# Kernel optimization log

Hardware: AMD Instinct MI355X
Metric: run time of the kernel (lower is better)

Reference implementation:

```python
import jax, jax.numpy as jnp
import numpy as np

TEMP = 1.0
EPS = 1e-6


def trop_linear(x, w, b, temp=TEMP):
    # x: (..., in), w: (out, in) -> (..., out)
    # y_i = temp * logsumexp_j((w_ij + x_j)/temp) + b_i  (soft tropical / max-plus)
    z = x[..., None, :] + w  # (..., out, in)
    y = temp * jax.nn.logsumexp(z / temp, axis=-1)
    return y + b


def trop_layernorm(x, weight, bias, eps=EPS):
    n = x.shape[-1]
    # torch.median returns the lower of the two middle elements for even n
    med = jnp.sort(x, axis=-1)[..., (n - 1) // 2][..., None]
    q75 = jnp.quantile(x, 0.75, axis=-1, keepdims=True)
    q25 = jnp.quantile(x, 0.25, axis=-1, keepdims=True)
    iqr = jnp.maximum(q75 - q25, eps)
    return (x - med) / iqr * weight + bias


def setup_inputs() -> dict:
    key = jax.random.key(0)
    ks = jax.random.split(key, 8)
    B, D_IN, D_H, D_OUT = 1024, 512, 512, 256
    return {
        "x": jax.random.normal(ks[0], (B, D_IN), dtype=jnp.float32),
        "w1": 0.1 * jax.random.normal(ks[1], (D_H, D_IN), dtype=jnp.float32),
        "b1": jnp.zeros((D_H,), dtype=jnp.float32),
        "ln1_w": jnp.ones((D_H,), dtype=jnp.float32),
        "ln1_b": jnp.zeros((D_H,), dtype=jnp.float32),
        "w2": 0.1 * jax.random.normal(ks[2], (D_H, D_H), dtype=jnp.float32),
        "b2": jnp.zeros((D_H,), dtype=jnp.float32),
        "ln2_w": jnp.ones((D_H,), dtype=jnp.float32),
        "ln2_b": jnp.zeros((D_H,), dtype=jnp.float32),
        "w3": 0.1 * jax.random.normal(ks[3], (D_OUT, D_H), dtype=jnp.float32),
        "b3": jnp.zeros((D_OUT,), dtype=jnp.float32),
    }


def reference(x, w1, b1, ln1_w, ln1_b, w2, b2, ln2_w, ln2_b, w3, b3):
    h = trop_linear(x, w1, b1)
    h = trop_layernorm(h, ln1_w, ln1_b)
    h = jnp.maximum(h, 0.0)  # TropicalActivation('relu', threshold=0)
    h = trop_linear(h, w2, b2)
    h = trop_layernorm(h, ln2_w, ln2_b)
    h = jnp.maximum(h, 0.0)
    return trop_linear(h, w3, b3)
```

## Files before the change

### kernel.cpp

```cpp
#include <hip/hip_runtime.h>
#include <math.h>


typedef _Float16 v8h __attribute__((ext_vector_type(8)));
typedef _Float16 v4h __attribute__((ext_vector_type(4)));
typedef float v4f __attribute__((ext_vector_type(4)));

#define ELS_STRIDE 528

__global__ __launch_bounds__(256) void expW_frag(const float* __restrict__ w1,
                                                 const float* __restrict__ w2,
                                                 const float* __restrict__ w3,
                                                 _Float16* __restrict__ Ef) {
    int u = blockIdx.x * 256 + threadIdx.x;
    int lane = u & 63, t = (u >> 6) & 15, S = u >> 10;
    int r = lane & 15, q = lane >> 4;
    const float* w; int tile;
    if (S < 32)      { w = w1; tile = S; }
    else if (S < 64) { w = w2; tile = S - 32; }
    else             { w = w3; tile = S - 64; }
    const float* src = w + (tile * 16 + r) * 512 + t * 32 + q * 8;
    float4 a = *reinterpret_cast<const float4*>(src);
    float4 b = *reinterpret_cast<const float4*>(src + 4);
    v8h o;
    o[0] = (_Float16)__expf(a.x); o[1] = (_Float16)__expf(a.y);
    o[2] = (_Float16)__expf(a.z); o[3] = (_Float16)__expf(a.w);
    o[4] = (_Float16)__expf(b.x); o[5] = (_Float16)__expf(b.y);
    o[6] = (_Float16)__expf(b.z); o[7] = (_Float16)__expf(b.w);
    *reinterpret_cast<v8h*>(Ef + u * 8) = o;
}

__device__ __forceinline__ void load_areg(const _Float16* Els, int lane, v8h* areg) {
    const int r = lane & 15, q = lane >> 4;
    const _Float16* ap = Els + (r & 3) * ELS_STRIDE + q * 8;
#pragma unroll
    for (int t = 0; t < 16; ++t)
        areg[t] = *reinterpret_cast<const v8h*>(ap + t * 32);
}

template <int NSUB>
__device__ __forceinline__ void gemm_frag(const _Float16* __restrict__ Bf,
                                          int s0, int lane,
                                          const v8h* areg, v4f* acc) {
    const _Float16* bp = Bf + lane * 8;
    v8h bb[4][NSUB];
#pragma unroll
    for (int p = 0; p < 3; ++p)
#pragma unroll
        for (int s = 0; s < NSUB; ++s)
            bb[p][s] = *reinterpret_cast<const v8h*>(bp + ((s0 + s) * 16 + p) * 512);
#pragma unroll
    for (int s = 0; s < NSUB; ++s) acc[s] = (v4f){0.f, 0.f, 0.f, 0.f};
#pragma unroll
    for (int t = 0; t < 16; ++t) {
        if (t + 3 < 16) {
#pragma unroll
            for (int s = 0; s < NSUB; ++s)
                bb[(t + 3) & 3][s] =
                    *reinterpret_cast<const v8h*>(bp + ((s0 + s) * 16 + t + 3) * 512);
        }
#pragma unroll
        for (int s = 0; s < NSUB; ++s)
            acc[s] = __builtin_amdgcn_mfma_f32_16x16x32_f16(areg[t], bb[t & 3][s],
                                                            acc[s], 0, 0, 0);
    }
}

__device__ __forceinline__ void ln_row(const float* hbuf,
                                       const float* __restrict__ lw,
                                       const float* __restrict__ lb,
                                       _Float16* Els, float* crow,
                                       int w, int lane) {
    float h[8], v[8];
    {
        const float* hp = hbuf + w * 512 + lane * 8;
        float4 a = *reinterpret_cast<const float4*>(hp);
        float4 b = *reinterpret_cast<const float4*>(hp + 4);
        h[0] = a.x; h[1] = a.y; h[2] = a.z; h[3] = a.w;
        h[4] = b.x; h[5] = b.y; h[6] = b.z; h[7] = b.w;
#pragma unroll
        for (int j = 0; j < 8; ++j) v[j] = h[j];
    }
#pragma unroll
    for (int k = 2; k <= 512; k <<= 1) {
#pragma unroll
        for (int jj = 256; jj > 0; jj >>= 1) {
            if (jj >= k) continue;
            if (jj >= 8) {
                int lm = jj >> 3;
#pragma unroll
                for (int j = 0; j < 8; ++j) {
                    float pv = __shfl_xor(v[j], lm);
                    bool up = ((((lane << 3) | j) & k) == 0);
                    bool low = ((lane & lm) == 0);
                    v[j] = (up == low) ? fminf(v[j], pv) : fmaxf(v[j], pv);
                }
            } else {
#pragma unroll
                for (int j = 0; j < 8; ++j) {
                    if (j & jj) continue;
                    int jh = j | jj;
                    bool up = ((((lane << 3) | j) & k) == 0);
                    float a = v[j], c = v[jh];
                    float lo = fminf(a, c), hi = fmaxf(a, c);
                    v[j] = up ? lo : hi;
                    v[jh] = up ? hi : lo;
                }
            }
        }
    }
    float s127 = __shfl(v[7], 15);
    float s128 = __shfl(v[0], 16);
    float med  = __shfl(v[7], 31);
    float s383 = __shfl(v[7], 47);
    float s384 = __shfl(v[0], 48);
    float q25 = s127 + 0.75f * (s128 - s127);
    float q75 = s383 + 0.25f * (s384 - s383);
    float inv = 1.0f / fmaxf(q75 - q25, 1e-6f);

    float y[8], cm = 0.0f;
    {
        const float4* lw4 = reinterpret_cast<const float4*>(lw + lane * 8);
        const float4* lb4 = reinterpret_cast<const float4*>(lb + lane * 8);
        float4 wa = lw4[0], wb = lw4[1], ba = lb4[0], bbv = lb4[1];
        float lwv[8] = {wa.x, wa.y, wa.z, wa.w, wb.x, wb.y, wb.z, wb.w};
        float lbv[8] = {ba.x, ba.y, ba.z, ba.w, bbv.x, bbv.y, bbv.z, bbv.w};
#pragma unroll
        for (int j = 0; j < 8; ++j) {
            y[j] = fmaxf((h[j] - med) * inv * lwv[j] + lbv[j], 0.0f);
            cm = fmaxf(cm, y[j]);
        }
    }
#pragma unroll
    for (int s = 32; s > 0; s >>= 1) cm = fmaxf(cm, __shfl_xor(cm, s));
    {
        v8h o;
#pragma unroll
        for (int j = 0; j < 8; ++j) o[j] = (_Float16)__expf(y[j] - cm);
        *reinterpret_cast<v8h*>(&Els[w * ELS_STRIDE + lane * 8]) = o;
    }
    if (lane == 0) crow[w] = cm;
}

__global__ __launch_bounds__(512, 2) void fused_rows(
    const float* __restrict__ x,
    const float* __restrict__ b1,
    const float* __restrict__ ln1w, const float* __restrict__ ln1b,
    const float* __restrict__ b2,
    const float* __restrict__ ln2w, const float* __restrict__ ln2b,
    const float* __restrict__ b3,
    const _Float16* __restrict__ Ew,
    float* __restrict__ out)
{
    __shared__ _Float16 Els[4 * ELS_STRIDE];
    __shared__ float hbuf[4 * 512];
    __shared__ float crow[4];

    const int tid = threadIdx.x;
    const int lane = tid & 63;
    const int w = tid >> 6;
    const int r = lane & 15, q = lane >> 4;
    const int blk = blockIdx.x;

    {
        int row = tid >> 7, col = (tid & 127) * 4;
        float4 a = *reinterpret_cast<const float4*>(x + blk * 2048 + row * 512 + col);
        v4h o;
        o[0] = (_Float16)__expf(a.x); o[1] = (_Float16)__expf(a.y);
        o[2] = (_Float16)__expf(a.z); o[3] = (_Float16)__expf(a.w);
        *reinterpret_cast<v4h*>(&Els[row * ELS_STRIDE + col]) = o;
    }
    __syncthreads();

    v8h areg[16];
    v4f acc[4];

    load_areg(Els, lane, areg);
    gemm_frag<4>(Ew, w * 4, lane, areg, acc);
    if (q == 0) {
#pragma unroll
        for (int s = 0; s < 4; ++s) {
            int col = (w * 4 + s) * 16 + r;
            float bb = b1[col];
#pragma unroll
            for (int t = 0; t < 4; ++t)
                hbuf[t * 512 + col] = __logf(acc[s][t]) + bb;
        }
    }
    __syncthreads();
    if (w < 4) ln_row(hbuf, ln1w, ln1b, Els, crow, w, lane);
    __syncthreads();

    load_areg(Els, lane, areg);
    gemm_frag<4>(Ew + 262144, w * 4, lane, areg, acc);
    if (q == 0) {
#pragma unroll
        for (int s = 0; s < 4; ++s) {
            int col = (w * 4 + s) * 16 + r;
            float bb = b2[col];
#pragma unroll
            for (int t = 0; t < 4; ++t)
                hbuf[t * 512 + col] = __logf(acc[s][t]) + bb;
        }
    }
    __syncthreads();
    if (w < 4) ln_row(hbuf, ln2w, ln2b, Els, crow, w, lane);
    __syncthreads();

    load_areg(Els, lane, areg);
    gemm_frag<2>(Ew + 524288, w * 2, lane, areg, acc);
    if (q == 0) {
#pragma unroll
        for (int s = 0; s < 2; ++s) {
            int col = (w * 2 + s) * 16 + r;
            float bb = b3[col];
#pragma unroll
            for (int t = 0; t < 4; ++t)
                out[(blk * 4 + t) * 256 + col] = __logf(acc[s][t]) + crow[t] + bb;
        }
    }
}

extern "C" void kernel_launch(void* const* d_in, const int* in_sizes, int n_in,
                              void* d_out, int out_size, void* d_ws, size_t ws_size,
                              hipStream_t stream) {
    const float* x    = (const float*)d_in[0];
    const float* w1   = (const float*)d_in[1];
    const float* b1   = (const float*)d_in[2];
    const float* ln1w = (const float*)d_in[3];
    const float* ln1b = (const float*)d_in[4];
    const float* w2   = (const float*)d_in[5];
    const float* b2   = (const float*)d_in[6];
    const float* ln2w = (const float*)d_in[7];
    const float* ln2b = (const float*)d_in[8];
    const float* w3   = (const float*)d_in[9];
    const float* b3   = (const float*)d_in[10];
    float* out = (float*)d_out;

    _Float16* Ew = (_Float16*)d_ws;

    expW_frag<<<320, 256, 0, stream>>>(w1, w2, w3, Ew);
    fused_rows<<<256, 512, 0, stream>>>(x, b1, ln1w, ln1b, b2, ln2w, ln2b,
                                        b3, Ew, out);
}
```

Baseline: 101.0 us.

## Switch exp-domain tropical GEMMs from fp16 to fp8 MFMA with scaling

Exponentiated weights and activations are now stored as packed fp8 instead of fp16, and the fp8 16x16x32 MFMA is used in place of the fp16 one. This halves the bytes read per weight fragment and per shared-memory A fragment. The B-fragment prefetch ring is also deepened from 3 to 8 tiles. Activations are pre-scaled (x4 and x64) to stay inside the fp8 range; the offset cancels through the shift-invariant layernorm and is subtracted in the final bias. The cost is a large loss of mantissa precision, which could break the accuracy tolerance.

```diff
diff --git a/kernel.cpp b/kernel.cpp
--- a/kernel.cpp
+++ b/kernel.cpp
@@ -2,16 +2,21 @@
 #include <math.h>
 
 
-typedef _Float16 v8h __attribute__((ext_vector_type(8)));
-typedef _Float16 v4h __attribute__((ext_vector_type(4)));
 typedef float v4f __attribute__((ext_vector_type(4)));
 
-#define ELS_STRIDE 528
+#define ELS_B 528
+#define LN64f 4.1588830833596715f
+
+__device__ __forceinline__ int pk4_fp8(float a, float b, float c, float d) {
+    int p = __builtin_amdgcn_cvt_pk_fp8_f32(a, b, 0, 0);
+    p = __builtin_amdgcn_cvt_pk_fp8_f32(c, d, p, 1);
+    return p;
+}
 
 __global__ __launch_bounds__(256) void expW_frag(const float* __restrict__ w1,
                                                  const float* __restrict__ w2,
                                                  const float* __restrict__ w3,
-                                                 _Float16* __restrict__ Ef) {
+                                                 uint8_t* __restrict__ Ef) {
     int u = blockIdx.x * 256 + threadIdx.x;
     int lane = u & 63, t = (u >> 6) & 15, S = u >> 10;
     int r = lane & 15, q = lane >> 4;
@@ -22,54 +27,55 @@
     const float* src = w + (tile * 16 + r) * 512 + t * 32 + q * 8;
     float4 a = *reinterpret_cast<const float4*>(src);
     float4 b = *reinterpret_cast<const float4*>(src + 4);
-    v8h o;
-    o[0] = (_Float16)__expf(a.x); o[1] = (_Float16)__expf(a.y);
-    o[2] = (_Float16)__expf(a.z); o[3] = (_Float16)__expf(a.w);
-    o[4] = (_Float16)__expf(b.x); o[5] = (_Float16)__expf(b.y);
-    o[6] = (_Float16)__expf(b.z); o[7] = (_Float16)__expf(b.w);
-    *reinterpret_cast<v8h*>(Ef + u * 8) = o;
-}
-
-__device__ __forceinline__ void load_areg(const _Float16* Els, int lane, v8h* areg) {
-    const int r = lane & 15, q = lane >> 4;
-    const _Float16* ap = Els + (r & 3) * ELS_STRIDE + q * 8;
+    int2 o;
+    o.x = pk4_fp8(__expf(a.x), __expf(a.y), __expf(a.z), __expf(a.w));
+    o.y = pk4_fp8(__expf(b.x), __expf(b.y), __expf(b.z), __expf(b.w));
+    *reinterpret_cast<int2*>(Ef + u * 8) = o;
+}
+
+__device__ __forceinline__ void load_areg(const uint8_t* Els, int lane, long* areg) {
+    const uint8_t* ap = Els + (lane & 3) * ELS_B + ((lane >> 4) & 3) * 8;
 #pragma unroll
     for (int t = 0; t < 16; ++t)
-        areg[t] = *reinterpret_cast<const v8h*>(ap + t * 32);
+        areg[t] = *reinterpret_cast<const long*>(ap + t * 32);
 }
 
 template <int NSUB>
-__device__ __forceinline__ void gemm_frag(const _Float16* __restrict__ Bf,
+__device__ __forceinline__ void gemm_frag(const uint8_t* __restrict__ Bf,
                                           int s0, int lane,
-                                          const v8h* areg, v4f* acc) {
-    const _Float16* bp = Bf + lane * 8;
-    v8h bb[4][NSUB];
-#pragma unroll
-    for (int p = 0; p < 3; ++p)
+                                          const long* areg, v4f* acc) {
+    const uint8_t* bp = Bf + lane * 8;
+    long bb[8][NSUB];
+#pragma unroll
+    for (int p = 0; p < 8; ++p)
 #pragma unroll
         for (int s = 0; s < NSUB; ++s)
-            bb[p][s] = *reinterpret_cast<const v8h*>(bp + ((s0 + s) * 16 + p) * 512);
+            bb[p][s] = *reinterpret_cast<const long*>(bp + ((s0 + s) * 16 + p) * 512);
 #pragma unroll
     for (int s = 0; s < NSUB; ++s) acc[s] = (v4f){0.f, 0.f, 0.f, 0.f};
 #pragma unroll
     for (int t = 0; t < 16; ++t) {
-        if (t + 3 < 16) {
+        long a = areg[t];
+        long bcur[NSUB];
+#pragma unroll
+        for (int s = 0; s < NSUB; ++s) bcur[s] = bb[t & 7][s];
+        if (t < 8) {
 #pragma unroll
             for (int s = 0; s < NSUB; ++s)
-                bb[(t + 3) & 3][s] =
-                    *reinterpret_cast<const v8h*>(bp + ((s0 + s) * 16 + t + 3) * 512);
+                bb[t & 7][s] =
+                    *reinterpret_cast<const long*>(bp + ((s0 + s) * 16 + t + 8) * 512);
         }
 #pragma unroll
         for (int s = 0; s < NSUB; ++s)
-            acc[s] = __builtin_amdgcn_mfma_f32_16x16x32_f16(areg[t], bb[t & 3][s],
-                                                            acc[s], 0, 0, 0);
+            acc[s] = __builtin_amdgcn_mfma_f32_16x16x32_fp8_fp8(a, bcur[s],
+                                                                acc[s], 0, 0, 0);
     }
 }
 
 __device__ __forceinline__ void ln_row(const float* hbuf,
                                        const float* __restrict__ lw,
                                        const float* __restrict__ lb,
-                                       _Float16* Els, float* crow,
+                                       uint8_t* Els, float* crow,
                                        int w, int lane) {
     float h[8], v[8];
     {
@@ -134,10 +140,13 @@
 #pragma unroll
     for (int s = 32; s > 0; s >>= 1) cm = fmaxf(cm, __shfl_xor(cm, s));
     {
-        v8h o;
-#pragma unroll
-        for (int j = 0; j < 8; ++j) o[j] = (_Float16)__expf(y[j] - cm);
-        *reinterpret_cast<v8h*>(&Els[w * ELS_STRIDE + lane * 8]) = o;
+        float e[8];
+#pragma unroll
+        for (int j = 0; j < 8; ++j) e[j] = 64.0f * __expf(y[j] - cm);
+        int2 o;
+        o.x = pk4_fp8(e[0], e[1], e[2], e[3]);
+        o.y = pk4_fp8(e[4], e[5], e[6], e[7]);
+        *reinterpret_cast<int2*>(&Els[w * ELS_B + lane * 8]) = o;
     }
     if (lane == 0) crow[w] = cm;
 }
@@ -149,10 +158,10 @@
     const float* __restrict__ b2,
     const float* __restrict__ ln2w, const float* __restrict__ ln2b,
     const float* __restrict__ b3,
-    const _Float16* __restrict__ Ew,
+    const uint8_t* __restrict__ Ew,
     float* __restrict__ out)
 {
-    __shared__ _Float16 Els[4 * ELS_STRIDE];
+    __shared__ uint8_t Els[4 * ELS_B];
     __shared__ float hbuf[4 * 512];
     __shared__ float crow[4];
 
@@ -165,14 +174,13 @@
     {
         int row = tid >> 7, col = (tid & 127) * 4;
         float4 a = *reinterpret_cast<const float4*>(x + blk * 2048 + row * 512 + col);
-        v4h o;
-        o[0] = (_Float16)__expf(a.x); o[1] = (_Float16)__expf(a.y);
-        o[2] = (_Float16)__expf(a.z); o[3] = (_Float16)__expf(a.w);
-        *reinterpret_cast<v4h*>(&Els[row * ELS_STRIDE + col]) = o;
-    }
-    __syncthreads();
-
-    v8h areg[16];
+        *reinterpret_cast<int*>(&Els[row * ELS_B + col]) =
+            pk4_fp8(4.0f * __expf(a.x), 4.0f * __expf(a.y),
+                    4.0f * __expf(a.z), 4.0f * __expf(a.w));
+    }
+    __syncthreads();
+
+    long areg[16];
     v4f acc[4];
 
     load_areg(Els, lane, areg);
@@ -213,7 +221,7 @@
 #pragma unroll
         for (int s = 0; s < 2; ++s) {
             int col = (w * 2 + s) * 16 + r;
-            float bb = b3[col];
+            float bb = b3[col] - LN64f;
 #pragma unroll
             for (int t = 0; t < 4; ++t)
                 out[(blk * 4 + t) * 256 + col] = __logf(acc[s][t]) + crow[t] + bb;
@@ -237,7 +245,7 @@
     const float* b3   = (const float*)d_in[10];
     float* out = (float*)d_out;
 
-    _Float16* Ew = (_Float16*)d_ws;
+    uint8_t* Ew = (uint8_t*)d_ws;
 
     expW_frag<<<320, 256, 0, stream>>>(w1, w2, w3, Ew);
     fused_rows<<<256, 512, 0, stream>>>(x, b1, ln1w, ln1b, b2, ln2w, ln2b,
```

After: 97.99 us. -3.0%, faster.
